# Kernel tuning notes

Measured on AMD Instinct MI355X. Metric: run time of the kernel, lower is better.

The kernel has to match this reference:

```python
import jax, jax.numpy as jnp
import numpy as np
from jax import lax

B, T, D, N = 64, 4096, 256, 64


def setup_inputs() -> dict:
    key = jax.random.key(0)
    ks = jax.random.split(key, 3)
    return {
        "x": jax.random.normal(ks[0], (B, T, D), dtype=jnp.float32),
        "mask": jnp.ones((B, T), dtype=bool),
        "W": jax.random.normal(ks[1], (D, N), dtype=jnp.float32) * (1.0 / np.sqrt(D)),
        "b": jnp.zeros((N,), dtype=jnp.float32),
        "trans": jax.random.normal(ks[2], (N, N), dtype=jnp.float32) * 0.1,
        "left_boundary": jnp.zeros((N,), dtype=jnp.float32),
        "right_boundary": jnp.zeros((N,), dtype=jnp.float32),
    }


def _viterbi_decode(potentials, lens, trans):
    # potentials: [B, T, N]; lens: [B] int32; trans: [N, N]
    Tt = potentials.shape[1]

    def fwd_step(state, inp):
        pot_t, t = inp  # pot_t: [B, N], t scalar time index (1..T-1)
        scores = state[:, :, None] + trans[None, :, :]        # [B, N_prev, N_cur]
        bp = jnp.argmax(scores, axis=1).astype(jnp.int32)      # [B, N]
        new_state = pot_t + jnp.max(scores, axis=1)            # [B, N]
        valid = (t < lens)[:, None]                            # carry state past length
        return jnp.where(valid, new_state, state), bp

    pots_t = jnp.swapaxes(potentials, 0, 1)  # [T, B, N]
    final_state, bps = lax.scan(fwd_step, pots_t[0], (pots_t[1:], jnp.arange(1, Tt)))
    last_tag = jnp.argmax(final_state, axis=1).astype(jnp.int32)  # [B]

    def bwd_step(tag, inp):
        bp, t = inp  # bp: [B, N] backpointers for time t+1; t in 0..T-2
        prev = jnp.take_along_axis(bp, tag[:, None], axis=1)[:, 0]
        new_tag = jnp.where(t < lens - 1, prev, last_tag)
        return new_tag, new_tag

    _, tags = lax.scan(bwd_step, last_tag, (bps, jnp.arange(Tt - 1)), reverse=True)
    # tags: [T-1, B], position t holds decoded tag at time t
    decoded = jnp.concatenate([tags.T, last_tag[:, None]], axis=1)  # [B, T]
    return decoded


def reference(x, mask, W, b, trans, left_boundary, right_boundary):
    # projection (use_kernel=True)
    pot = jnp.einsum("btd,dn->btn", x, W) + b  # [B, T, N]
    # boundary potentials (use_boundary=True): added at fixed first/last timestep
    pot = pot.at[:, 0, :].add(left_boundary)
    pot = pot.at[:, -1, :].add(right_boundary)
    lens = jnp.sum(mask.astype(jnp.int32), axis=1)  # [B]
    decoded = _viterbi_decode(pot, lens, trans)
    return decoded, pot, lens, trans
```

## Files before the change

kernel.cpp:

```cpp
#include <hip/hip_runtime.h>

#define B_ 64
#define T_ 4096
#define D_ 256
#define N_ 64

typedef float f32x16 __attribute__((ext_vector_type(16)));

__global__ __launch_bounds__(64) void k_misc(const unsigned char* __restrict__ mask,
                                             const float* __restrict__ trans,
                                             float* __restrict__ out_lens,
                                             float* __restrict__ out_trans,
                                             int* __restrict__ lens_i) {
  int blk = blockIdx.x, lane = threadIdx.x;
  if (blk < B_) {
    int probe = (int)mask[0] + (int)mask[1] + (int)mask[2] + (int)mask[3];
    int cnt = 0;
    if (probe >= 2) {
      const unsigned char* row = mask + (size_t)blk * T_;
      for (int i = lane; i < T_; i += 64) cnt += row[i] ? 1 : 0;
    } else {
      const int* rowi = (const int*)mask + (size_t)blk * T_;
      for (int i = lane; i < T_; i += 64) cnt += rowi[i] ? 1 : 0;
    }
    #pragma unroll
    for (int off = 32; off > 0; off >>= 1) cnt += __shfl_down(cnt, off, 64);
    if (lane == 0) { out_lens[blk] = (float)cnt; lens_i[blk] = cnt; }
  } else {
    int base = (blk - B_) * 1024;
    for (int i = lane; i < 1024; i += 64) out_trans[base + i] = trans[base + i];
  }
}

__global__ __launch_bounds__(256, 2) void k_gemm(const float* __restrict__ x,
                                                 const float* __restrict__ W,
                                                 const float* __restrict__ bias,
                                                 const float* __restrict__ lb,
                                                 const float* __restrict__ rb,
                                                 float* __restrict__ pot) {
  __shared__ float xs[64 * D_];
  int tid = threadIdx.x;
  int wid = tid >> 6, lane = tid & 63;
  size_t row0 = (size_t)blockIdx.x * 64;

  const float* xb = x + row0 * D_;
  #pragma unroll
  for (int i = 0; i < 16; ++i) {
    int r = wid * 16 + i;
    float4 v = *reinterpret_cast<const float4*>(xb + (size_t)r * D_ + lane * 4);
    *reinterpret_cast<float4*>(&xs[r * D_ + lane * 4]) = v;
  }
  __syncthreads();

  float bv = bias[lane];
  float lbv = lb[lane];
  float rbv = rb[lane];

  float acc[16];
  #pragma unroll
  for (int r = 0; r < 16; ++r) {
    int t = (int)((row0 + wid * 16 + r) & (T_ - 1));
    float a = bv;
    if (t == 0)      a += lbv;
    if (t == T_ - 1) a += rbv;
    acc[r] = a;
  }

  #pragma unroll
  for (int c = 0; c < 4; ++c) {
    float w[64];
    #pragma unroll
    for (int k = 0; k < 64; ++k) w[k] = W[(size_t)(c * 64 + k) * N_ + lane];
    #pragma unroll
    for (int r = 0; r < 16; ++r) {
      const float4* xr = reinterpret_cast<const float4*>(&xs[(wid * 16 + r) * D_ + c * 64]);
      #pragma unroll
      for (int q = 0; q < 16; ++q) {
        float4 xv = xr[q];
        acc[r] += xv.x * w[q * 4 + 0];
        acc[r] += xv.y * w[q * 4 + 1];
        acc[r] += xv.z * w[q * 4 + 2];
        acc[r] += xv.w * w[q * 4 + 3];
      }
    }
  }

  #pragma unroll
  for (int r = 0; r < 16; ++r)
    pot[(row0 + wid * 16 + r) * N_ + lane] = acc[r];
}

#define FWD_STEP(TIDX, PREG)                                                      \
  {                                                                               \
    float pot_t = PREG;                                                           \
    int tp = (TIDX) + 4; if (tp > T_ - 1) tp = T_ - 1;                            \
    PREG = pb[(size_t)tp * N_ + lane];                                            \
    float m[64];                                                                  \
    _Pragma("unroll")                                                             \
    for (int g = 0; g < 16; ++g) {                                                \
      float4 s4 = st4v[g];                                                        \
      float2 ca = make_float2(s4.x, s4.y) + t2[2 * g];                            \
      float2 cb = make_float2(s4.z, s4.w) + t2[2 * g + 1];                        \
      m[4 * g + 0] = ca.x; m[4 * g + 1] = ca.y;                                   \
      m[4 * g + 2] = cb.x; m[4 * g + 3] = cb.y;                                   \
    }                                                                             \
    float r1[22];                                                                 \
    _Pragma("unroll")                                                             \
    for (int i = 0; i < 21; ++i)                                                  \
      r1[i] = fmaxf(fmaxf(m[3 * i], m[3 * i + 1]), m[3 * i + 2]);                 \
    r1[21] = m[63];                                                               \
    float r2[8];                                                                  \
    _Pragma("unroll")                                                             \
    for (int i = 0; i < 7; ++i)                                                   \
      r2[i] = fmaxf(fmaxf(r1[3 * i], r1[3 * i + 1]), r1[3 * i + 2]);              \
    r2[7] = r1[21];                                                               \
    float r3a = fmaxf(fmaxf(r2[0], r2[1]), r2[2]);                                \
    float r3b = fmaxf(fmaxf(r2[3], r2[4]), r2[5]);                                \
    float r3c = fmaxf(r2[6], r2[7]);                                              \
    float best = fmaxf(fmaxf(r3a, r3b), r3c);                                     \
    float ns = pot_t + best;                                                      \
    state = ((TIDX) < len_b) ? ns : state;                                        \
    sb[(size_t)(TIDX) * N_ + lane] = state;                                       \
    __builtin_amdgcn_wave_barrier();                                              \
    st[lane] = state;                                                             \
    __builtin_amdgcn_wave_barrier();                                              \
  }

__global__ __launch_bounds__(64, 1) void k_fwd_states(const float* __restrict__ pot,
                                                      const float* __restrict__ trans,
                                                      const int* __restrict__ lens_i,
                                                      float* __restrict__ states,
                                                      float* __restrict__ fstate) {
  int b = blockIdx.x, lane = threadIdx.x;
  __shared__ float4 st4v[16];
  float* st = (float*)st4v;

  float2 t2[32];
  #pragma unroll
  for (int p = 0; p < 32; ++p)
    t2[p] = make_float2(trans[(2 * p) * N_ + lane], trans[(2 * p + 1) * N_ + lane]);

  const float* pb = pot + (size_t)b * T_ * N_;
  float* sb = states + (size_t)b * T_ * N_;
  int len_b = lens_i[b];

  float state = pb[lane];
  st[lane] = state;
  sb[lane] = state;
  __builtin_amdgcn_wave_barrier();

  float p0 = pb[1 * N_ + lane];
  float p1 = pb[2 * N_ + lane];
  float p2 = pb[3 * N_ + lane];
  float p3 = pb[4 * N_ + lane];

  int t = 1;
  for (; t + 3 <= T_ - 1; t += 4) {
    FWD_STEP(t + 0, p0);
    FWD_STEP(t + 1, p1);
    FWD_STEP(t + 2, p2);
    FWD_STEP(t + 3, p3);
  }
  FWD_STEP(t + 0, p0);
  FWD_STEP(t + 1, p1);
  FWD_STEP(t + 2, p2);

  fstate[b * N_ + lane] = state;
}

#define BP_CHUNK 64
__global__ __launch_bounds__(64, 2) void k_bp(const float* __restrict__ states,
                                              const float* __restrict__ trans,
                                              unsigned char* __restrict__ bp) {
  int nchunk = T_ / BP_CHUNK;
  int b = blockIdx.x / nchunk;
  int chunk = blockIdx.x - b * nchunk;
  int lane = threadIdx.x;

  float tcol[64];
  #pragma unroll
  for (int p = 0; p < 64; ++p) tcol[p] = trans[p * N_ + lane];

  int t0 = chunk * BP_CHUNK;
  int tstart = (t0 == 0) ? 1 : t0;
  int tend = t0 + BP_CHUNK;

  for (int t = tstart; t < tend; ++t) {
    const f32x16* sr = reinterpret_cast<const f32x16*>(states + ((size_t)b * T_ + (t - 1)) * N_);
    f32x16 s0 = sr[0], s1 = sr[1], s2 = sr[2], s3 = sr[3];

    float c[64];
    #pragma unroll
    for (int j = 0; j < 16; ++j) {
      c[j]      = s0[j] + tcol[j];
      c[16 + j] = s1[j] + tcol[16 + j];
      c[32 + j] = s2[j] + tcol[32 + j];
      c[48 + j] = s3[j] + tcol[48 + j];
    }

    float r1[22];
    #pragma unroll
    for (int i = 0; i < 21; ++i) r1[i] = fmaxf(fmaxf(c[3 * i], c[3 * i + 1]), c[3 * i + 2]);
    r1[21] = c[63];
    float r2[8];
    #pragma unroll
    for (int i = 0; i < 7; ++i) r2[i] = fmaxf(fmaxf(r1[3 * i], r1[3 * i + 1]), r1[3 * i + 2]);
    r2[7] = r1[21];
    float r3a = fmaxf(fmaxf(r2[0], r2[1]), r2[2]);
    float r3b = fmaxf(fmaxf(r2[3], r2[4]), r2[5]);
    float r3c = fmaxf(r2[6], r2[7]);
    float best = fmaxf(fmaxf(r3a, r3b), r3c);

    int bpi = 63;
    #pragma unroll
    for (int p = 62; p >= 0; --p) bpi = (c[p] == best) ? p : bpi;

    bp[((size_t)b * T_ + t) * N_ + lane] = (unsigned char)bpi;
  }
}

__global__ __launch_bounds__(64, 1) void k_bwd(const unsigned char* __restrict__ bp,
                                               const float* __restrict__ fstate,
                                               const int* __restrict__ lens_i,
                                               float* __restrict__ decoded) {
  int b = blockIdx.x, lane = threadIdx.x;

  __shared__ float fv[64];
  __shared__ int sh_tag;
  fv[lane] = fstate[b * N_ + lane];
  __syncthreads();
  if (lane == 0) {
    float best = fv[0]; int tg = 0;
    for (int i = 1; i < 64; ++i) if (fv[i] > best) { best = fv[i]; tg = i; }
    sh_tag = tg;
  }
  __syncthreads();
  int s_last = __builtin_amdgcn_readfirstlane(sh_tag);
  int len_b = lens_i[b];

  const unsigned char* bpb = bp + (size_t)b * T_ * N_;
  float* dec = decoded + (size_t)b * T_;

  int s_tag = s_last;
  if (lane == 0) dec[T_ - 1] = (float)s_last;

  const int G = 32;
  int bufA[G], bufB[G];
  const int k0 = T_ - 1;
  #pragma unroll
  for (int i = 0; i < G; ++i) bufA[i] = (int)bpb[(size_t)(k0 - i) * N_ + lane];

  const int nrows = T_ - 1;
  const int groups = nrows / G;

  for (int g = 0; g < groups; ++g) {
    int kn = k0 - G * (g + 1);
    #pragma unroll
    for (int i = 0; i < G; ++i)
      bufB[i] = (kn - i >= 1) ? (int)bpb[(size_t)(kn - i) * N_ + lane] : 0;

    int kbase = k0 - G * g;
    #pragma unroll
    for (int i = 0; i < G; ++i) {
      int k = kbase - i;
      int prev = __builtin_amdgcn_readlane(bufA[i], s_tag);
      int t = k - 1;
      s_tag = (t < len_b - 1) ? prev : s_last;
      if (lane == 0) dec[t] = (float)s_tag;
    }
    #pragma unroll
    for (int i = 0; i < G; ++i) bufA[i] = bufB[i];
  }

  int kbase = k0 - G * groups;
  #pragma unroll
  for (int i = 0; i < G; ++i) {
    int k = kbase - i;
    if (k >= 1) {
      int prev = __builtin_amdgcn_readlane(bufA[i], s_tag);
      int t = k - 1;
      s_tag = (t < len_b - 1) ? prev : s_last;
      if (lane == 0) dec[t] = (float)s_tag;
    }
  }
}

extern "C" void kernel_launch(void* const* d_in, const int* in_sizes, int n_in,
                              void* d_out, int out_size, void* d_ws, size_t ws_size,
                              hipStream_t stream) {
  const float* x            = (const float*)d_in[0];
  const unsigned char* mask = (const unsigned char*)d_in[1];
  const float* W            = (const float*)d_in[2];
  const float* bias         = (const float*)d_in[3];
  const float* trans        = (const float*)d_in[4];
  const float* lb           = (const float*)d_in[5];
  const float* rb           = (const float*)d_in[6];

  float* out         = (float*)d_out;
  float* out_decoded = out;
  float* out_pot     = out + (size_t)B_ * T_;
  float* out_lens    = out_pot + (size_t)B_ * T_ * N_;
  float* out_trans   = out_lens + B_;

  const size_t bp_bytes   = (size_t)B_ * T_ * N_;
  const size_t fstate_off = bp_bytes;
  const size_t lens_off   = fstate_off + (size_t)B_ * N_ * 4;
  const size_t states_off = lens_off + 256;

  unsigned char* bp = (unsigned char*)d_ws;
  float* fstate     = (float*)((char*)d_ws + fstate_off);
  int*   lens_i     = (int*)((char*)d_ws + lens_off);
  float* states     = (float*)((char*)d_ws + states_off);

  k_misc<<<68, 64, 0, stream>>>(mask, trans, out_lens, out_trans, lens_i);
  k_gemm<<<(B_ * T_) / 64, 256, 0, stream>>>(x, W, bias, lb, rb, out_pot);
  k_fwd_states<<<B_, 64, 0, stream>>>(out_pot, trans, lens_i, states, fstate);
  k_bp<<<B_ * (T_ / BP_CHUNK), 64, 0, stream>>>(states, trans, bp);
  k_bwd<<<B_, 64, 0, stream>>>(bp, fstate, lens_i, out_decoded);
}
```

Measured before the change: 1.548 ms.

## Fuse backpointer argmax into sequential forward Viterbi kernel, drop states buffer

Computes the per-step argmax backpointer inside the forward recurrence with a pairwise value/index tree, writing byte backpointers directly. This removes the k_bp kernel and the full float states buffer, which was written by the forward pass and read back by k_bp. The cost is extra ALU work in the latency-bound single-wave-per-batch forward loop. That work sits off the state dependency chain, so it may fill idle issue slots, but it could also lengthen each step.

```diff
diff --git a/kernel.cpp b/kernel.cpp
--- a/kernel.cpp
+++ b/kernel.cpp
@@ -104,6 +104,7 @@
       m[4 * g + 0] = ca.x; m[4 * g + 1] = ca.y;                                   \
       m[4 * g + 2] = cb.x; m[4 * g + 3] = cb.y;                                   \
     }                                                                             \
+                                  \
     float r1[22];                                                                 \
     _Pragma("unroll")                                                             \
     for (int i = 0; i < 21; ++i)                                                  \
@@ -120,17 +121,51 @@
     float best = fmaxf(fmaxf(r3a, r3b), r3c);                                     \
     float ns = pot_t + best;                                                      \
     state = ((TIDX) < len_b) ? ns : state;                                        \
-    sb[(size_t)(TIDX) * N_ + lane] = state;                                       \
+         \
+    float v1[32]; int i1[32];                                                     \
+    _Pragma("unroll")                                                             \
+    for (int i = 0; i < 32; ++i) {                                                \
+      bool g = m[2 * i + 1] > m[2 * i];                                           \
+      v1[i] = g ? m[2 * i + 1] : m[2 * i];                                        \
+      i1[i] = g ? 2 * i + 1 : 2 * i;                                              \
+    }                                                                             \
+    float v2[16]; int i2[16];                                                     \
+    _Pragma("unroll")                                                             \
+    for (int i = 0; i < 16; ++i) {                                                \
+      bool g = v1[2 * i + 1] > v1[2 * i];                                         \
+      v2[i] = g ? v1[2 * i + 1] : v1[2 * i];                                      \
+      i2[i] = g ? i1[2 * i + 1] : i1[2 * i];                                      \
+    }                                                                             \
+    float v3[8]; int i3[8];                                                       \
+    _Pragma("unroll")                                                             \
+    for (int i = 0; i < 8; ++i) {                                                 \
+      bool g = v2[2 * i + 1] > v2[2 * i];                                         \
+      v3[i] = g ? v2[2 * i + 1] : v2[2 * i];                                      \
+      i3[i] = g ? i2[2 * i + 1] : i2[2 * i];                                      \
+    }                                                                             \
+    float v4[4]; int i4[4];                                                       \
+    _Pragma("unroll")                                                             \
+    for (int i = 0; i < 4; ++i) {                                                 \
+      bool g = v3[2 * i + 1] > v3[2 * i];                                         \
+      v4[i] = g ? v3[2 * i + 1] : v3[2 * i];                                      \
+      i4[i] = g ? i3[2 * i + 1] : i3[2 * i];                                      \
+    }                                                                             \
+    bool ga = v4[1] > v4[0];                                                      \
+    float va = ga ? v4[1] : v4[0]; int ia = ga ? i4[1] : i4[0];                    \
+    bool gb = v4[3] > v4[2];                                                      \
+    float vb = gb ? v4[3] : v4[2]; int ib = gb ? i4[3] : i4[2];                    \
+    int bpi = (vb > va) ? ib : ia;                                                \
+    bpb[(size_t)(TIDX) * N_ + lane] = (unsigned char)bpi;                         \
     __builtin_amdgcn_wave_barrier();                                              \
     st[lane] = state;                                                             \
     __builtin_amdgcn_wave_barrier();                                              \
   }
 
-__global__ __launch_bounds__(64, 1) void k_fwd_states(const float* __restrict__ pot,
-                                                      const float* __restrict__ trans,
-                                                      const int* __restrict__ lens_i,
-                                                      float* __restrict__ states,
-                                                      float* __restrict__ fstate) {
+__global__ __launch_bounds__(64, 1) void k_fwd_bp(const float* __restrict__ pot,
+                                                  const float* __restrict__ trans,
+                                                  const int* __restrict__ lens_i,
+                                                  unsigned char* __restrict__ bp,
+                                                  float* __restrict__ fstate) {
   int b = blockIdx.x, lane = threadIdx.x;
   __shared__ float4 st4v[16];
   float* st = (float*)st4v;
@@ -141,12 +176,11 @@
     t2[p] = make_float2(trans[(2 * p) * N_ + lane], trans[(2 * p + 1) * N_ + lane]);
 
   const float* pb = pot + (size_t)b * T_ * N_;
-  float* sb = states + (size_t)b * T_ * N_;
+  unsigned char* bpb = bp + (size_t)b * T_ * N_;
   int len_b = lens_i[b];
 
   float state = pb[lane];
   st[lane] = state;
-  sb[lane] = state;
   __builtin_amdgcn_wave_barrier();
 
   float p0 = pb[1 * N_ + lane];
@@ -166,57 +200,6 @@
   FWD_STEP(t + 2, p2);
 
   fstate[b * N_ + lane] = state;
-}
-
-#define BP_CHUNK 64
-__global__ __launch_bounds__(64, 2) void k_bp(const float* __restrict__ states,
-                                              const float* __restrict__ trans,
-                                              unsigned char* __restrict__ bp) {
-  int nchunk = T_ / BP_CHUNK;
-  int b = blockIdx.x / nchunk;
-  int chunk = blockIdx.x - b * nchunk;
-  int lane = threadIdx.x;
-
-  float tcol[64];
-  #pragma unroll
-  for (int p = 0; p < 64; ++p) tcol[p] = trans[p * N_ + lane];
-
-  int t0 = chunk * BP_CHUNK;
-  int tstart = (t0 == 0) ? 1 : t0;
-  int tend = t0 + BP_CHUNK;
-
-  for (int t = tstart; t < tend; ++t) {
-    const f32x16* sr = reinterpret_cast<const f32x16*>(states + ((size_t)b * T_ + (t - 1)) * N_);
-    f32x16 s0 = sr[0], s1 = sr[1], s2 = sr[2], s3 = sr[3];
-
-    float c[64];
-    #pragma unroll
-    for (int j = 0; j < 16; ++j) {
-      c[j]      = s0[j] + tcol[j];
-      c[16 + j] = s1[j] + tcol[16 + j];
-      c[32 + j] = s2[j] + tcol[32 + j];
-      c[48 + j] = s3[j] + tcol[48 + j];
-    }
-
-    float r1[22];
-    #pragma unroll
-    for (int i = 0; i < 21; ++i) r1[i] = fmaxf(fmaxf(c[3 * i], c[3 * i + 1]), c[3 * i + 2]);
-    r1[21] = c[63];
-    float r2[8];
-    #pragma unroll
-    for (int i = 0; i < 7; ++i) r2[i] = fmaxf(fmaxf(r1[3 * i], r1[3 * i + 1]), r1[3 * i + 2]);
-    r2[7] = r1[21];
-    float r3a = fmaxf(fmaxf(r2[0], r2[1]), r2[2]);
-    float r3b = fmaxf(fmaxf(r2[3], r2[4]), r2[5]);
-    float r3c = fmaxf(r2[6], r2[7]);
-    float best = fmaxf(fmaxf(r3a, r3b), r3c);
-
-    int bpi = 63;
-    #pragma unroll
-    for (int p = 62; p >= 0; --p) bpi = (c[p] == best) ? p : bpi;
-
-    bp[((size_t)b * T_ + t) * N_ + lane] = (unsigned char)bpi;
-  }
 }
 
 __global__ __launch_bounds__(64, 1) void k_bwd(const unsigned char* __restrict__ bp,
@@ -305,16 +288,13 @@
   const size_t bp_bytes   = (size_t)B_ * T_ * N_;
   const size_t fstate_off = bp_bytes;
   const size_t lens_off   = fstate_off + (size_t)B_ * N_ * 4;
-  const size_t states_off = lens_off + 256;
 
   unsigned char* bp = (unsigned char*)d_ws;
   float* fstate     = (float*)((char*)d_ws + fstate_off);
   int*   lens_i     = (int*)((char*)d_ws + lens_off);
-  float* states     = (float*)((char*)d_ws + states_off);
 
   k_misc<<<68, 64, 0, stream>>>(mask, trans, out_lens, out_trans, lens_i);
   k_gemm<<<(B_ * T_) / 64, 256, 0, stream>>>(x, W, bias, lb, rb, out_pot);
-  k_fwd_states<<<B_, 64, 0, stream>>>(out_pot, trans, lens_i, states, fstate);
-  k_bp<<<B_ * (T_ / BP_CHUNK), 64, 0, stream>>>(states, trans, bp);
+  k_fwd_bp<<<B_, 64, 0, stream>>>(out_pot, trans, lens_i, bp, fstate);
   k_bwd<<<B_, 64, 0, stream>>>(bp, fstate, lens_i, out_decoded);
 }
```

Result: slower. 2.684 ms (+73.4%).
